# Kernel optimization log

Hardware: AMD Instinct MI355X
Metric: run time of the kernel (lower is better)

## Reference

```python
import jax, jax.numpy as jnp
import numpy as np

N, T = 64, 256
V, E, K = 32000, 256, 128


def setup_inputs() -> dict:
    key = jax.random.key(0)
    ks = jax.random.split(key, 7)
    x = jax.random.randint(ks[0], (N, T), 0, V)
    embed_w = jax.random.normal(ks[1], (V, E), dtype=jnp.float32) * 0.02
    # nn.Linear(embed_dim, K*K, bias=False), weight.uniform_(-1, 1)
    trans_w = jax.random.uniform(ks[2], (K * K, E), dtype=jnp.float32, minval=-1.0, maxval=1.0)
    # nn.Linear(1, K): weight [K,1], bias [K]
    start_w = jax.random.normal(ks[3], (K, 1), dtype=jnp.float32)
    start_b = jax.random.normal(ks[4], (K,), dtype=jnp.float32) * 0.1
    # nn.Embedding(K, K) cluster embeddings
    emb_cluster_w = jax.random.normal(ks[5], (K, K), dtype=jnp.float32)
    # nn.Linear(K, vocab, bias=False), weight.uniform_(-1, 1) -> weight [V, K]
    emit_w = jax.random.uniform(ks[6], (V, K), dtype=jnp.float32, minval=-1.0, maxval=1.0)
    return {"x": x, "embed_w": embed_w, "trans_w": trans_w, "start_w": start_w,
            "start_b": start_b, "emb_cluster_w": emb_cluster_w, "emit_w": emit_w}


def reference(x, embed_w, trans_w, start_w, start_b, emb_cluster_w, emit_w):
    n, t = x.shape
    k = emb_cluster_w.shape[0]
    ex = embed_w[x]                                            # [N,T,E]
    # Emissions: log_softmax(emit(emb_cluster(i))) per cluster -> [K,V]
    log_emit = jax.nn.log_softmax(emb_cluster_w @ emit_w.T, axis=-1)
    log_emit_t = log_emit.T                                    # [V,K]
    # start(dummy): ones[N,1] @ W.T + b = W[:,0]+b, same per row
    pre = jax.nn.log_softmax(start_w[:, 0] + start_b)          # [K]
    pre = jnp.broadcast_to(pre, (n, k))
    xs = (jnp.swapaxes(ex[:, :-1, :], 0, 1),                   # [T-1,N,E]
          x[:, 1:].T)                                          # [T-1,N]
    def step(pre_alpha, inp):
        x_prev, w_t = inp
        tran = jax.nn.log_softmax((x_prev @ trans_w.T).reshape(n, k, k), axis=-1)
        cur = jax.nn.logsumexp(pre_alpha[:, :, None] + tran, axis=1)   # [N,K]
        cur = cur + log_emit_t[w_t]                            # add log p(w_t | state)
        return cur, None
    cur, _ = jax.lax.scan(step, pre, xs)
    return -jnp.mean(jax.nn.logsumexp(cur, axis=1))
```

## Files before the change

### kernel.cpp

```cpp
#include <hip/hip_runtime.h>
#include <cstdint>
#include <cstddef>

#define N_SEQ 64
#define T_LEN 256
#define VOCAB 32000
#define EDIM  256
#define KS    128
#define KK    16384
#define MROWS 16384
#define MREAL 16320
#define GPART 16

typedef short  short8  __attribute__((ext_vector_type(8)));
typedef float  floatx4 __attribute__((ext_vector_type(4)));
typedef int    intx8   __attribute__((ext_vector_type(8)));

#define LGKM_BARRIER() asm volatile("s_waitcnt lgkmcnt(0)\n\ts_barrier" ::: "memory")
#define LGKM_WAIT()    asm volatile("s_waitcnt lgkmcnt(0)" ::: "memory")

static __device__ __forceinline__ unsigned short f2bf(float f) {
  unsigned u = __float_as_uint(f);
  u += 0x7fffu + ((u >> 16) & 1u);
  return (unsigned short)(u >> 16);
}

static __device__ __forceinline__ void gl_lds16(const void* gptr, void* lptr) {
  __builtin_amdgcn_global_load_lds(
      (const __attribute__((address_space(1))) void*)gptr,
      (__attribute__((address_space(3))) void*)lptr, 16, 0, 0);
}

__global__ __launch_bounds__(128) void k_prep(const float* sw, const float* sb, float* pre0) {
  __shared__ float vals[KS];
  __shared__ float MM, LS;
  int tid = threadIdx.x;
  float v = sw[tid] + sb[tid];
  vals[tid] = v;
  __syncthreads();
  if (tid == 0) { float m = vals[0]; for (int i = 1; i < KS; ++i) m = fmaxf(m, vals[i]); MM = m; }
  __syncthreads();
  float e = __expf(v - MM);
  vals[tid] = e;
  __syncthreads();
  if (tid == 0) { float s = 0.f; for (int i = 0; i < KS; ++i) s += vals[i]; LS = MM + __logf(s); }
  __syncthreads();
  pre0[tid] = v - LS;
}

__global__ __launch_bounds__(256) void k_transcvt(const float* tw, unsigned short* tb) {
  int idx = blockIdx.x * 256 + threadIdx.x;
  if (idx >= (KK * EDIM) / 4) return;
  int row = idx >> 6, e4 = idx & 63;
  int rowp = ((row & 127) << 7) | (row >> 7);
  int e4s = (e4 & 0x31) | (((((e4 >> 1) & 7) ^ (rowp & 7))) << 1);
  float4 v = *(const float4*)&tw[(size_t)idx * 4];
  unsigned h0 = f2bf(v.x), h1 = f2bf(v.y), h2 = f2bf(v.z), h3 = f2bf(v.w);
  uint2 o; o.x = h0 | (h1 << 16); o.y = h2 | (h3 << 16);
  *(uint2*)&tb[(size_t)rowp * EDIM + e4s * 4] = o;
}

__global__ __launch_bounds__(256) void k_embed(const int* x, const float* ew, unsigned short* exb) {
  int m = blockIdx.x, e = threadIdx.x;
  int t = m >> 6, n = m & 63;
  float v = 0.f;
  if (m < MREAL) { int tok = x[n * T_LEN + t]; v = ew[(size_t)tok * EDIM + e]; }
  int es = (e & 0xC7) | ((((e >> 3) & 7) ^ (m & 7)) << 3);
  exb[(size_t)m * EDIM + es] = f2bf(v);
}

__global__ __launch_bounds__(256) void k_emitlogits(const float* ecl, const float* emw, float* C) {
  int v0 = blockIdx.x * 64, k0 = blockIdx.y * 64;
  int tid = threadIdx.x;
  __shared__ alignas(16) float At[64 * 17];
  __shared__ alignas(16) float Bt[64 * 17];
  int tx = tid & 15, ty = tid >> 4;
  int r = tid >> 2, q = tid & 3;
  float acc[4][4] = {};
  for (int d0 = 0; d0 < KS; d0 += 16) {
    float4 av = *(const float4*)&ecl[(size_t)(k0 + r) * KS + d0 + q * 4];
    float4 bv = *(const float4*)&emw[(size_t)(v0 + r) * KS + d0 + q * 4];
    __syncthreads();
    At[r * 17 + q * 4 + 0] = av.x; At[r * 17 + q * 4 + 1] = av.y;
    At[r * 17 + q * 4 + 2] = av.z; At[r * 17 + q * 4 + 3] = av.w;
    Bt[r * 17 + q * 4 + 0] = bv.x; Bt[r * 17 + q * 4 + 1] = bv.y;
    Bt[r * 17 + q * 4 + 2] = bv.z; Bt[r * 17 + q * 4 + 3] = bv.w;
    __syncthreads();
    #pragma unroll
    for (int dd = 0; dd < 16; ++dd) {
      float a[4], b[4];
      #pragma unroll
      for (int i = 0; i < 4; ++i) a[i] = At[(ty * 4 + i) * 17 + dd];
      #pragma unroll
      for (int i = 0; i < 4; ++i) b[i] = Bt[(tx * 4 + i) * 17 + dd];
      #pragma unroll
      for (int i = 0; i < 4; ++i)
        #pragma unroll
        for (int jj = 0; jj < 4; ++jj) acc[i][jj] += a[i] * b[jj];
    }
  }
  #pragma unroll
  for (int i = 0; i < 4; ++i) {
    float4 o; o.x = acc[i][0]; o.y = acc[i][1]; o.z = acc[i][2]; o.w = acc[i][3];
    *(float4*)&C[(size_t)(k0 + ty * 4 + i) * VOCAB + v0 + tx * 4] = o;
  }
}

__global__ __launch_bounds__(256) void k_lsec(const float* C, float* lseC) {
  int k = blockIdx.x, tid = threadIdx.x;
  __shared__ float sm[4], ss[4];
  const float* row = C + (size_t)k * VOCAB;
  float m = -1e30f;
  for (int v = tid; v < VOCAB; v += 256) m = fmaxf(m, row[v]);
  #pragma unroll
  for (int s = 1; s < 64; s <<= 1) m = fmaxf(m, __shfl_xor(m, s));
  if ((tid & 63) == 0) sm[tid >> 6] = m;
  __syncthreads();
  m = fmaxf(fmaxf(sm[0], sm[1]), fmaxf(sm[2], sm[3]));
  float sum = 0.f;
  for (int v = tid; v < VOCAB; v += 256) sum += __expf(row[v] - m);
  #pragma unroll
  for (int s = 1; s < 64; s <<= 1) sum += __shfl_xor(sum, s);
  if ((tid & 63) == 0) ss[tid >> 6] = sum;
  __syncthreads();
  if (tid == 0) lseC[k] = m + __logf(ss[0] + ss[1] + ss[2] + ss[3]);
}

__global__ __launch_bounds__(128) void k_emis(const int* x, const float* C, const float* lseC,
                                              float* emis, float* emax) {
  int t = blockIdx.x + 1;
  int n = blockIdx.y;
  int k = threadIdx.x;
  __shared__ float red[2];
  int w = x[n * T_LEN + t];
  float v = C[(size_t)k * VOCAB + w] - lseC[k];
  emis[(size_t)((n << 8) + t) * KS + k] = v;
  float m = v;
  #pragma unroll
  for (int s = 1; s < 64; s <<= 1) m = fmaxf(m, __shfl_xor(m, s));
  if ((k & 63) == 0) red[k >> 6] = m;
  __syncthreads();
  if (k == 0) emax[n * T_LEN + t] = fmaxf(red[0], red[1]);
}

__global__ __launch_bounds__(256) void k_comb(const float* srowP, float* srowR,
                                              int m_base, int Rcap, int rows) {
  int id = blockIdx.x * 256 + threadIdx.x;
  if (id >= rows * KS) return;
  float s = 0.f;
  #pragma unroll
  for (int g = 0; g < GPART; ++g) s += srowP[(size_t)g * Rcap * KS + id];
  srowR[(size_t)m_base * KS + id] = 1.0f / s;
}

static __device__ __forceinline__ void scan_load_S(const unsigned char* Sbase,
                                                   int l15, int kg, intx8 (&sf)[8]) {
  #pragma unroll
  for (int q = 0; q < 8; ++q) {
    const uint4* p = (const uint4*)(Sbase + (size_t)(q * 16 + l15) * 128 + kg * 32);
    uint4 a = p[0], b = p[1];
    sf[q][0] = a.x; sf[q][1] = a.y; sf[q][2] = a.z; sf[q][3] = a.w;
    sf[q][4] = b.x; sf[q][5] = b.y; sf[q][6] = b.z; sf[q][7] = b.w;
  }
}

static __device__ __forceinline__ void scan_step(
    int t, int t0, int t1, int n, int l15, int kg, bool do_u,
    const unsigned char* Sc, const float* srowR, const float* emis, const float* emax,
    unsigned char* uL8, intx8 (&sf)[8], intx8& uf,
    float (&em)[8], float (&rs)[8], float& exR,
    float (&pre)[8], float& M) {
  const float SCALE = 4096.0f;
  const float LNS = 8.317766167f;
  floatx4 cz = {0.f, 0.f, 0.f, 0.f};
  float cv[8];
  #pragma unroll
  for (int q = 0; q < 8; ++q) {
    floatx4 d = __builtin_amdgcn_mfma_scale_f32_16x16x128_f8f6f4(
        uf, sf[q], cz, 0, 0, 0, 0x7F7F7F7F, 0, 0x7F7F7F7F);
    cv[q] = d[0];
  }
  int tp = (t + 2 < t1) ? (t + 2) : (t1 - 1);
  scan_load_S(Sc + (size_t)((tp - t0) * 64 + n) * KK, l15, kg, sf);
  float c0 = __uint_as_float(__builtin_amdgcn_readfirstlane(__float_as_uint(cv[0])));
  float Mn = M + exR + __logf(c0) - LNS;
  #pragma unroll
  for (int q = 0; q < 8; ++q) pre[q] = M - LNS + __logf(cv[q]) + em[q];
  M = Mn;
  if (do_u) {
    #pragma unroll
    for (int q = 0; q < 8; ++q) {
      float up = __expf(pre[q] - M) * rs[q] * SCALE;
      int pk = __builtin_amdgcn_cvt_pk_fp8_f32(up, up, 0, 0);
      uL8[q * 16 + l15] = (unsigned char)(pk & 0xff);
    }
  }
  em[0] = emis[(size_t)((n << 8) + tp) * KS + 0 * 16 + l15];
  em[1] = emis[(size_t)((n << 8) + tp) * KS + 1 * 16 + l15];
  em[2] = emis[(size_t)((n << 8) + tp) * KS + 2 * 16 + l15];
  em[3] = emis[(size_t)((n << 8) + tp) * KS + 3 * 16 + l15];
  em[4] = emis[(size_t)((n << 8) + tp) * KS + 4 * 16 + l15];
  em[5] = emis[(size_t)((n << 8) + tp) * KS + 5 * 16 + l15];
  em[6] = emis[(size_t)((n << 8) + tp) * KS + 6 * 16 + l15];
  em[7] = emis[(size_t)((n << 8) + tp) * KS + 7 * 16 + l15];
  #pragma unroll
  for (int q = 0; q < 8; ++q) rs[q] = srowR[(size_t)(tp * 64 + n) * KS + q * 16 + l15];
  exR = emax[n * T_LEN + tp];
  if (do_u) {
    LGKM_WAIT();
    uint4 ua = *(const uint4*)&uL8[kg * 32];
    uint4 ub = *(const uint4*)&uL8[kg * 32 + 16];
    uf[0] = ua.x; uf[1] = ua.y; uf[2] = ua.z; uf[3] = ua.w;
    uf[4] = ub.x; uf[5] = ub.y; uf[6] = ub.z; uf[7] = ub.w;
  }
}

__global__ __launch_bounds__(256, 2) void k_fused(
    const unsigned short* exb, const unsigned short* trb,
    unsigned char* Sg, float* srowP, int m_base, int Rcap,
    const unsigned char* Ss, const float* srowR, const float* emis,
    const float* emax, const float* pre0, float* alphaG, float* nll,
    int t0s, int tcs) {
  __shared__ alignas(16) unsigned short As[128 * 64];
  __shared__ alignas(16) unsigned short Bs[128 * 64];
  __shared__ alignas(16) unsigned char uL8[KS];

  if (blockIdx.x < 64) {
    if (tcs <= 0 || threadIdx.x >= 64) return;
    int n = blockIdx.x;
    int L = threadIdx.x, l15 = L & 15, kg = L >> 4;
    const float SCALE = 4096.0f;
    int t1 = t0s + tcs;
    const float* a0 = (t0s == 1) ? pre0 : (alphaG + (size_t)n * KS);
    float pre[8];
    #pragma unroll
    for (int q = 0; q < 8; ++q) pre[q] = a0[q * 16 + l15];
    float mx = pre[0];
    #pragma unroll
    for (int q = 1; q < 8; ++q) mx = fmaxf(mx, pre[q]);
    #pragma unroll
    for (int s2 = 1; s2 < 16; s2 <<= 1) mx = fmaxf(mx, __shfl_xor(mx, s2));
    float M = mx;
    #pragma unroll
    for (int q = 0; q < 8; ++q) {
      float r0 = srowR[(size_t)((t0s - 1) * 64 + n) * KS + q * 16 + l15];
      float up = __expf(pre[q] - M) * r0 * SCALE;
      int pk = __builtin_amdgcn_cvt_pk_fp8_f32(up, up, 0, 0);
      uL8[q * 16 + l15] = (unsigned char)(pk & 0xff);
    }
    LGKM_WAIT();
    intx8 uf;
    {
      uint4 ua = *(const uint4*)&uL8[kg * 32];
      uint4 ub = *(const uint4*)&uL8[kg * 32 + 16];
      uf[0] = ua.x; uf[1] = ua.y; uf[2] = ua.z; uf[3] = ua.w;
      uf[4] = ub.x; uf[5] = ub.y; uf[6] = ub.z; uf[7] = ub.w;
    }
    intx8 sfA[8], sfB[8];
    scan_load_S(Ss + (size_t)n * KK, l15, kg, sfA);
    int tB = (t0s + 1 < t1) ? (t0s + 1) : (t1 - 1);
    scan_load_S(Ss + (size_t)((tB - t0s) * 64 + n) * KK, l15, kg, sfB);
    float emA[8], rsA[8], emB[8], rsB[8];
    #pragma unroll
    for (int q = 0; q < 8; ++q) {
      emA[q] = emis[(size_t)((n << 8) + t0s) * KS + q * 16 + l15];
      rsA[q] = srowR[(size_t)(t0s * 64 + n) * KS + q * 16 + l15];
      emB[q] = emis[(size_t)((n << 8) + tB) * KS + q * 16 + l15];
      rsB[q] = srowR[(size_t)(tB * 64 + n) * KS + q * 16 + l15];
    }
    float exA = emax[n * T_LEN + t0s];
    float exB = emax[n * T_LEN + tB];
    int t = t0s;
    for (;;) {
      scan_step(t, t0s, t1, n, l15, kg, (t + 1 < t1), Ss, srowR, emis, emax,
                uL8, sfA, uf, emA, rsA, exA, pre, M);
      ++t; if (t >= t1) break;
      scan_step(t, t0s, t1, n, l15, kg, (t + 1 < t1), Ss, srowR, emis, emax,
                uL8, sfB, uf, emB, rsB, exB, pre, M);
      ++t; if (t >= t1) break;
    }
    #pragma unroll
    for (int q = 0; q < 8; ++q) alphaG[(size_t)n * KS + q * 16 + l15] = pre[q];
    if (t1 == T_LEN) {
      float m2 = pre[0];
      #pragma unroll
      for (int q = 1; q < 8; ++q) m2 = fmaxf(m2, pre[q]);
      #pragma unroll
      for (int s2 = 1; s2 < 16; s2 <<= 1) m2 = fmaxf(m2, __shfl_xor(m2, s2));
      float e = 0.f;
      #pragma unroll
      for (int q = 0; q < 8; ++q) e += __expf(pre[q] - m2);
      #pragma unroll
      for (int s2 = 1; s2 < 16; s2 <<= 1) e += __shfl_xor(e, s2);
      if (L == 0) nll[n] = m2 + __logf(e);
    }
    return;
  }

  int g = blockIdx.x - 64;
  int bx = g >> 4, grp = g & 15;
  int tid = threadIdx.x, wv = tid >> 6, ln = tid & 63;
  int wc = wv & 1, wm = wv >> 1;
  int m0 = m_base + bx * 128;
  int lr = ln & 15, lk = (ln >> 4) * 8;
  int lg = ln >> 4;
  floatx4 sacc[4][4] = {};
  for (int byi = 0; byi < 8; ++byi) {
    int by = grp * 8 + byi;
    int c0 = by * 128;
    floatx4 acc[4][4] = {};
    for (int k0 = 0; k0 < EDIM; k0 += 64) {
      #pragma unroll
      for (int r = 0; r < 4; ++r) {
        int chunk = (wv * 4 + r) * 64 + ln;
        int row = chunk >> 3, c8 = chunk & 7;
        gl_lds16(&exb[(size_t)(m0 + row) * EDIM + k0 + c8 * 8], &As[(wv * 4 + r) * 512]);
        gl_lds16(&trb[(size_t)(c0 + row) * EDIM + k0 + c8 * 8], &Bs[(wv * 4 + r) * 512]);
      }
      __syncthreads();
      #pragma unroll
      for (int kk = 0; kk < 64; kk += 32) {
        int sw = ((((kk + lk) >> 3) ^ (lr & 7)) << 3);
        short8 af[4], bf[4];
        #pragma unroll
        for (int f = 0; f < 4; ++f)
          af[f] = *(const short8*)&As[(wm * 64 + f * 16 + lr) * 64 + sw];
        #pragma unroll
        for (int f = 0; f < 4; ++f)
          bf[f] = *(const short8*)&Bs[(wc * 64 + f * 16 + lr) * 64 + sw];
        #pragma unroll
        for (int fc = 0; fc < 4; ++fc)
          #pragma unroll
          for (int fm = 0; fm < 4; ++fm)
            acc[fc][fm] = __builtin_amdgcn_mfma_f32_16x16x32_bf16(bf[fc], af[fm], acc[fc][fm], 0, 0, 0);
      }
      LGKM_BARRIER();
    }
    unsigned char* Ts = (unsigned char*)As;
    #pragma unroll
    for (int fc = 0; fc < 4; ++fc) {
      #pragma unroll
      for (int fm = 0; fm < 4; ++fm) {
        floatx4 a = acc[fc][fm];
        float e0 = __expf(a[0]), e1 = __expf(a[1]), e2 = __expf(a[2]), e3 = __expf(a[3]);
        int p = __builtin_amdgcn_cvt_pk_fp8_f32(e0, e1, 0, 0);
        p = __builtin_amdgcn_cvt_pk_fp8_f32(e2, e3, p, 1);
        int mloc = wm * 64 + fm * 16 + lr;
        int cl = wc * 64 + fc * 16 + lg * 4;
        *(int*)&Ts[mloc * 128 + (cl ^ ((mloc & 7) << 4))] = p;
        sacc[fc][fm][0] += e0; sacc[fc][fm][1] += e1;
        sacc[fc][fm][2] += e2; sacc[fc][fm][3] += e3;
      }
    }
    LGKM_BARRIER();
    #pragma unroll
    for (int r = 0; r < 4; ++r) {
      int seg = r * 256 + tid;
      int mloc = seg >> 3, s = seg & 7;
      uint4 v = *(const uint4*)&Ts[mloc * 128 + ((s ^ (mloc & 7)) << 4)];
      *(uint4*)&Sg[(size_t)(bx * 128 + mloc) * KK + c0 + s * 16] = v;
    }
    LGKM_BARRIER();
  }
  #pragma unroll
  for (int fc = 0; fc < 4; ++fc) {
    #pragma unroll
    for (int fm = 0; fm < 4; ++fm) {
      int mloc = bx * 128 + wm * 64 + fm * 16 + lr;
      int i = wc * 64 + fc * 16 + lg * 4;
      *(floatx4*)&srowP[((size_t)grp * Rcap + mloc) * KS + i] = sacc[fc][fm];
    }
  }
}

__global__ __launch_bounds__(64) void k_final(const float* nll, float* out) {
  int tid = threadIdx.x;
  float v = nll[tid];
  #pragma unroll
  for (int s = 1; s < 64; s <<= 1) v += __shfl_xor(v, s);
  if (tid == 0) out[0] = -v / 64.0f;
}

extern "C" void kernel_launch(void* const* d_in, const int* in_sizes, int n_in,
                              void* d_out, int out_size, void* d_ws, size_t ws_size,
                              hipStream_t stream) {
  const int*   x       = (const int*)d_in[0];
  const float* embed_w = (const float*)d_in[1];
  const float* trans_w = (const float*)d_in[2];
  const float* start_w = (const float*)d_in[3];
  const float* start_b = (const float*)d_in[4];
  const float* ecl     = (const float*)d_in[5];
  const float* emw     = (const float*)d_in[6];

  char* w = (char*)d_ws;
  size_t off = 0;
  auto alloc = [&](size_t bytes) -> char* {
    char* p = w + off;
    off = (off + bytes + 255) & ~(size_t)255;
    return p;
  };
  float*          pre0   = (float*)alloc(KS * 4);
  float*          lseC   = (float*)alloc(KS * 4);
  float*          nll    = (float*)alloc(N_SEQ * 4);
  float*          alphaG = (float*)alloc((size_t)N_SEQ * KS * 4);
  float*          emax   = (float*)alloc((size_t)N_SEQ * T_LEN * 4);
  unsigned short* trb    = (unsigned short*)alloc((size_t)KK * EDIM * 2);
  unsigned short* exb    = (unsigned short*)alloc((size_t)MROWS * EDIM * 2);
  float*          emis   = (float*)alloc((size_t)N_SEQ * T_LEN * KS * 4);
  float*          srowR  = (float*)alloc((size_t)MROWS * KS * 4);
  char* region = w + off;
  size_t avail = (ws_size > off) ? (ws_size - off) : 0;
  float* C = (float*)region;

  int Tc = 2;
  for (int c = 2; c <= 64; c += 2)
    if ((size_t)c * 64 * 40960 <= avail) Tc = c;
  int Rcap = Tc * 64;
  unsigned char* S0    = (unsigned char*)region;
  unsigned char* S1    = (unsigned char*)(region + (size_t)Rcap * KK);
  float*         srowP = (float*)(region + (size_t)2 * Rcap * KK);

  hipLaunchKernelGGL(k_prep,       dim3(1),        dim3(128), 0, stream, start_w, start_b, pre0);
  hipLaunchKernelGGL(k_transcvt,   dim3(4096),     dim3(256), 0, stream, trans_w, trb);
  hipLaunchKernelGGL(k_embed,      dim3(16384),    dim3(256), 0, stream, x, embed_w, exb);
  hipLaunchKernelGGL(k_emitlogits, dim3(500, 2),   dim3(256), 0, stream, ecl, emw, C);
  hipLaunchKernelGGL(k_lsec,       dim3(128),      dim3(256), 0, stream, C, lseC);
  hipLaunchKernelGGL(k_emis,       dim3(255, 64),  dim3(128), 0, stream, x, C, lseC, emis, emax);

  int ct0[140], ctc[140], nc = 0;
  {
    int t0 = 1;
    while (t0 < T_LEN) {
      int tc = T_LEN - t0; if (tc > Tc) tc = Tc;
      ct0[nc] = t0; ctc[nc] = tc; ++nc; t0 += tc;
    }
  }
  for (int c = 0; c <= nc; ++c) {
    bool hasG = (c < nc), hasS = (c > 0);
    int gx = 0, m_base = 0;
    if (hasG) { gx = (ctc[c] * 64 + 127) / 128; m_base = (ct0[c] - 1) * 64; }
    unsigned char* Sg = (c & 1) ? S1 : S0;
    unsigned char* Ssc = ((c - 1) & 1) ? S1 : S0;
    int t0s = hasS ? ct0[c - 1] : 0;
    int tcs = hasS ? ctc[c - 1] : 0;
    hipLaunchKernelGGL(k_fused, dim3(64 + gx * 16), dim3(256), 0, stream,
                       exb, trb, Sg, srowP, m_base, Rcap,
                       Ssc, srowR, emis, emax, pre0, alphaG, nll, t0s, tcs);
    if (hasG)
      hipLaunchKernelGGL(k_comb, dim3(gx * 64), dim3(256), 0, stream,
                         srowP, srowR, m_base, Rcap, gx * 128);
  }
  hipLaunchKernelGGL(k_final, dim3(1), dim3(64), 0, stream, nll, (float*)d_out);
}
```

Baseline: 583.4 us.

## Fold emission weights and row reciprocals into precomputed scan multipliers

The combine kernel now also computes, per (t,n,k), a multiplier exp(emis - emax) * rowRecip * scale and stores it in a new workspace buffer. The serial scan step then forms the next fp8 vector directly as cv * w / c0, using a fast reciprocal instead of a log then exp per element. Only the running scale M still takes a log, and the full log-alpha is rebuilt at the end of each chunk. This shortens the latency-bound serial recurrence and halves its per-step global loads, at the cost of an extra buffer write in the combine kernel and some change in rounding.

```diff
diff --git a/kernel.cpp b/kernel.cpp
--- a/kernel.cpp
+++ b/kernel.cpp
@@ -23,6 +23,14 @@
   unsigned u = __float_as_uint(f);
   u += 0x7fffu + ((u >> 16) & 1u);
   return (unsigned short)(u >> 16);
+}
+
+static __device__ __forceinline__ float fast_rcp(float x) {
+#if __has_builtin(__builtin_amdgcn_rcpf)
+  return __builtin_amdgcn_rcpf(x);
+#else
+  return 1.0f / x;
+#endif
 }
 
 static __device__ __forceinline__ void gl_lds16(const void* gptr, void* lptr) {
@@ -143,14 +151,25 @@
   if (k == 0) emax[n * T_LEN + t] = fmaxf(red[0], red[1]);
 }
 
-__global__ __launch_bounds__(256) void k_comb(const float* srowP, float* srowR,
+__global__ __launch_bounds__(256) void k_comb(const float* srowP, float* srowR, float* wcomb,
+                                              const float* emis, const float* emax,
                                               int m_base, int Rcap, int rows) {
   int id = blockIdx.x * 256 + threadIdx.x;
   if (id >= rows * KS) return;
   float s = 0.f;
   #pragma unroll
   for (int g = 0; g < GPART; ++g) s += srowP[(size_t)g * Rcap * KS + id];
-  srowR[(size_t)m_base * KS + id] = 1.0f / s;
+  float r = 1.0f / s;
+  srowR[(size_t)m_base * KS + id] = r;
+  int m = m_base + (id >> 7);
+  int t = m >> 6, n = m & 63, k = id & 127;
+  float wv = 0.f;
+  if (t >= 1) {
+    float e  = emis[(size_t)((n << 8) + t) * KS + k];
+    float ex = emax[n * T_LEN + t];
+    wv = __expf(e - ex) * r * 4096.0f;
+  }
+  wcomb[(size_t)m_base * KS + id] = wv;
 }
 
 static __device__ __forceinline__ void scan_load_S(const unsigned char* Sbase,
@@ -164,13 +183,11 @@
   }
 }
 
-static __device__ __forceinline__ void scan_step(
-    int t, int t0, int t1, int n, int l15, int kg, bool do_u,
-    const unsigned char* Sc, const float* srowR, const float* emis, const float* emax,
+static __device__ __forceinline__ void scan_step2(
+    int t, int t0, int tLast, int n, int l15, int kg,
+    const unsigned char* Sc, const float* wcomb, const float* emax,
     unsigned char* uL8, intx8 (&sf)[8], intx8& uf,
-    float (&em)[8], float (&rs)[8], float& exR,
-    float (&pre)[8], float& M) {
-  const float SCALE = 4096.0f;
+    float (&wv)[8], float& exR, float& M) {
   const float LNS = 8.317766167f;
   floatx4 cz = {0.f, 0.f, 0.f, 0.f};
   float cv[8];
@@ -180,34 +197,22 @@
         uf, sf[q], cz, 0, 0, 0, 0x7F7F7F7F, 0, 0x7F7F7F7F);
     cv[q] = d[0];
   }
-  int tp = (t + 2 < t1) ? (t + 2) : (t1 - 1);
+  int tp = t + 2; if (tp > tLast) tp = tLast;
   scan_load_S(Sc + (size_t)((tp - t0) * 64 + n) * KK, l15, kg, sf);
   float c0 = __uint_as_float(__builtin_amdgcn_readfirstlane(__float_as_uint(cv[0])));
-  float Mn = M + exR + __logf(c0) - LNS;
-  #pragma unroll
-  for (int q = 0; q < 8; ++q) pre[q] = M - LNS + __logf(cv[q]) + em[q];
-  M = Mn;
-  if (do_u) {
-    #pragma unroll
-    for (int q = 0; q < 8; ++q) {
-      float up = __expf(pre[q] - M) * rs[q] * SCALE;
-      int pk = __builtin_amdgcn_cvt_pk_fp8_f32(up, up, 0, 0);
-      uL8[q * 16 + l15] = (unsigned char)(pk & 0xff);
-    }
-  }
-  em[0] = emis[(size_t)((n << 8) + tp) * KS + 0 * 16 + l15];
-  em[1] = emis[(size_t)((n << 8) + tp) * KS + 1 * 16 + l15];
-  em[2] = emis[(size_t)((n << 8) + tp) * KS + 2 * 16 + l15];
-  em[3] = emis[(size_t)((n << 8) + tp) * KS + 3 * 16 + l15];
-  em[4] = emis[(size_t)((n << 8) + tp) * KS + 4 * 16 + l15];
-  em[5] = emis[(size_t)((n << 8) + tp) * KS + 5 * 16 + l15];
-  em[6] = emis[(size_t)((n << 8) + tp) * KS + 6 * 16 + l15];
-  em[7] = emis[(size_t)((n << 8) + tp) * KS + 7 * 16 + l15];
-  #pragma unroll
-  for (int q = 0; q < 8; ++q) rs[q] = srowR[(size_t)(tp * 64 + n) * KS + q * 16 + l15];
+  float rc = fast_rcp(c0);
+  #pragma unroll
+  for (int q = 0; q < 8; ++q) {
+    float up = cv[q] * wv[q] * rc;
+    int pk = __builtin_amdgcn_cvt_pk_fp8_f32(up, up, 0, 0);
+    uL8[q * 16 + l15] = (unsigned char)(pk & 0xff);
+  }
+  M += exR + __logf(c0) - LNS;
+  #pragma unroll
+  for (int q = 0; q < 8; ++q) wv[q] = wcomb[(size_t)(tp * 64 + n) * KS + q * 16 + l15];
   exR = emax[n * T_LEN + tp];
-  if (do_u) {
-    LGKM_WAIT();
+  LGKM_WAIT();
+  {
     uint4 ua = *(const uint4*)&uL8[kg * 32];
     uint4 ub = *(const uint4*)&uL8[kg * 32 + 16];
     uf[0] = ua.x; uf[1] = ua.y; uf[2] = ua.z; uf[3] = ua.w;
@@ -218,9 +223,9 @@
 __global__ __launch_bounds__(256, 2) void k_fused(
     const unsigned short* exb, const unsigned short* trb,
     unsigned char* Sg, float* srowP, int m_base, int Rcap,
-    const unsigned char* Ss, const float* srowR, const float* emis,
-    const float* emax, const float* pre0, float* alphaG, float* nll,
-    int t0s, int tcs) {
+    const unsigned char* Ss, const float* srowR, const float* wcomb,
+    const float* emis, const float* emax, const float* pre0,
+    float* alphaG, float* nll, int t0s, int tcs) {
   __shared__ alignas(16) unsigned short As[128 * 64];
   __shared__ alignas(16) unsigned short Bs[128 * 64];
   __shared__ alignas(16) unsigned char uL8[KS];
@@ -230,7 +235,8 @@
     int n = blockIdx.x;
     int L = threadIdx.x, l15 = L & 15, kg = L >> 4;
     const float SCALE = 4096.0f;
-    int t1 = t0s + tcs;
+    const float LNS = 8.317766167f;
+    int t1 = t0s + tcs, tLast = t1 - 1;
     const float* a0 = (t0s == 1) ? pre0 : (alphaG + (size_t)n * KS);
     float pre[8];
     #pragma unroll
@@ -258,26 +264,38 @@
     }
     intx8 sfA[8], sfB[8];
     scan_load_S(Ss + (size_t)n * KK, l15, kg, sfA);
-    int tB = (t0s + 1 < t1) ? (t0s + 1) : (t1 - 1);
+    int tB = (t0s + 1 < t1) ? (t0s + 1) : tLast;
     scan_load_S(Ss + (size_t)((tB - t0s) * 64 + n) * KK, l15, kg, sfB);
-    float emA[8], rsA[8], emB[8], rsB[8];
+    float wA[8], wB[8];
     #pragma unroll
     for (int q = 0; q < 8; ++q) {
-      emA[q] = emis[(size_t)((n << 8) + t0s) * KS + q * 16 + l15];
-      rsA[q] = srowR[(size_t)(t0s * 64 + n) * KS + q * 16 + l15];
-      emB[q] = emis[(size_t)((n << 8) + tB) * KS + q * 16 + l15];
-      rsB[q] = srowR[(size_t)(tB * 64 + n) * KS + q * 16 + l15];
+      wA[q] = wcomb[(size_t)(t0s * 64 + n) * KS + q * 16 + l15];
+      wB[q] = wcomb[(size_t)(tB * 64 + n) * KS + q * 16 + l15];
     }
     float exA = emax[n * T_LEN + t0s];
     float exB = emax[n * T_LEN + tB];
     int t = t0s;
-    for (;;) {
-      scan_step(t, t0s, t1, n, l15, kg, (t + 1 < t1), Ss, srowR, emis, emax,
-                uL8, sfA, uf, emA, rsA, exA, pre, M);
-      ++t; if (t >= t1) break;
-      scan_step(t, t0s, t1, n, l15, kg, (t + 1 < t1), Ss, srowR, emis, emax,
-                uL8, sfB, uf, emB, rsB, exB, pre, M);
-      ++t; if (t >= t1) break;
+    while (t < tLast) {
+      scan_step2(t, t0s, tLast, n, l15, kg, Ss, wcomb, emax, uL8, sfA, uf, wA, exA, M);
+      ++t;
+      if (t >= tLast) break;
+      scan_step2(t, t0s, tLast, n, l15, kg, Ss, wcomb, emax, uL8, sfB, uf, wB, exB, M);
+      ++t;
+    }
+    {
+      floatx4 cz = {0.f, 0.f, 0.f, 0.f};
+      float cv[8];
+      #pragma unroll
+      for (int q = 0; q < 8; ++q) {
+        floatx4 d = __builtin_amdgcn_mfma_scale_f32_16x16x128_f8f6f4(
+            uf, sfA[q], cz, 0, 0, 0, 0x7F7F7F7F, 0, 0x7F7F7F7F);
+        cv[q] = d[0];
+      }
+      #pragma unroll
+      for (int q = 0; q < 8; ++q) {
+        float em = emis[(size_t)((n << 8) + tLast) * KS + q * 16 + l15];
+        pre[q] = M - LNS + __logf(cv[q]) + em;
+      }
     }
     #pragma unroll
     for (int q = 0; q < 8; ++q) alphaG[(size_t)n * KS + q * 16 + l15] = pre[q];
@@ -408,6 +426,7 @@
   unsigned short* exb    = (unsigned short*)alloc((size_t)MROWS * EDIM * 2);
   float*          emis   = (float*)alloc((size_t)N_SEQ * T_LEN * KS * 4);
   float*          srowR  = (float*)alloc((size_t)MROWS * KS * 4);
+  float*          wcomb  = (float*)alloc((size_t)MROWS * KS * 4);
   char* region = w + off;
   size_t avail = (ws_size > off) ? (ws_size - off) : 0;
   float* C = (float*)region;
@@ -445,10 +464,10 @@
     int tcs = hasS ? ctc[c - 1] : 0;
     hipLaunchKernelGGL(k_fused, dim3(64 + gx * 16), dim3(256), 0, stream,
                        exb, trb, Sg, srowP, m_base, Rcap,
-                       Ssc, srowR, emis, emax, pre0, alphaG, nll, t0s, tcs);
+                       Ssc, srowR, wcomb, emis, emax, pre0, alphaG, nll, t0s, tcs);
     if (hasG)
       hipLaunchKernelGGL(k_comb, dim3(gx * 64), dim3(256), 0, stream,
-                         srowP, srowR, m_base, Rcap, gx * 128);
+                         srowP, srowR, wcomb, emis, emax, m_base, Rcap, gx * 128);
   }
   hipLaunchKernelGGL(k_final, dim3(1), dim3(64), 0, stream, nll, (float*)d_out);
 }
```

Result: no change. 576.3 us (-1.2%).
